# Kernel tuning notes

Hardware: AMD Instinct MI355X
Metric: run time of the kernel (lower is better)

The kernel has to match this reference:

```python
import jax, jax.numpy as jnp
import numpy as np

N_ORDERS = 4  # edge groups processed sequentially by EmulsionConv


def setup_inputs() -> dict:
    key = jax.random.key(0)
    ks = jax.random.split(key, 12)
    N, E, D_IN, H, D_OUT, ED = 50000, 800000, 10, 64, 10, 1
    s = 0.1
    return {
        "x": jax.random.normal(ks[0], (N, D_IN), jnp.float32),
        "edge_index": jax.random.randint(ks[1], (2, E), 0, N, jnp.int32),
        "edge_features": jax.random.normal(ks[2], (E, ED), jnp.float32),
        "lin0_w": jax.random.normal(ks[3], (D_IN, H), jnp.float32) * s,
        "lin0_b": jnp.zeros((H,), jnp.float32),
        "lin1_w": jax.random.normal(ks[4], (H, H), jnp.float32) * s,
        "lin1_b": jnp.zeros((H,), jnp.float32),
        "lin2_w": jax.random.normal(ks[5], (H, H), jnp.float32) * s,
        "lin2_b": jnp.zeros((H,), jnp.float32),
        "em_w": jax.random.normal(ks[6], (3, 2 * H + ED, H), jnp.float32) * s,
        "em_b": jnp.zeros((3, H), jnp.float32),
        "ec_w": jax.random.normal(ks[7], (3, 2 * H, H), jnp.float32) * s,
        "ec_b": jnp.zeros((3, H), jnp.float32),
        "out_w": jax.random.normal(ks[8], (H, D_OUT), jnp.float32) * s,
        "out_b": jnp.zeros((D_OUT,), jnp.float32),
    }


def _emulsion_conv(x, edge_index, edge_features, w, b):
    # Sequential per-order gather -> MLP message -> scatter-add; direction=0 (aggregate at source).
    N = x.shape[0]
    E = edge_index.shape[1]
    per = E // N_ORDERS
    for i in range(N_ORDERS):
        sl = slice(i * per, (i + 1) * per)
        src = edge_index[0, sl]
        dst = edge_index[1, sl]
        x_j = x[src]  # [per, H]
        x_i = x[dst]  # [per, H]
        msg = jnp.concatenate([x_i, x_j - x_i, edge_features[sl]], axis=1)
        msg = jax.nn.relu(msg @ w + b)
        agg = jax.ops.segment_sum(msg, src, num_segments=N)
        x = (x + agg) / 2.0
    return x


def _edge_conv(x, edge_index, w, b):
    # EdgeConv: nn([x_i, x_j - x_i]) with max aggregation at target nodes.
    N = x.shape[0]
    src, dst = edge_index[0], edge_index[1]
    x_i = x[dst]
    x_j = x[src]
    msg = jax.nn.relu(jnp.concatenate([x_i, x_j - x_i], axis=1) @ w + b)
    agg = jax.ops.segment_max(msg, dst, num_segments=N)
    return jnp.where(jnp.isfinite(agg), agg, 0.0)  # empty segments -> 0


def reference(x, edge_index, edge_features,
              lin0_w, lin0_b, lin1_w, lin1_b, lin2_w, lin2_b,
              em_w, em_b, ec_w, ec_b, out_w, out_b):
    lin_ws = [lin0_w, lin1_w, lin2_w]
    lin_bs = [lin0_b, lin1_b, lin2_b]
    for i in range(3):
        x = jax.nn.relu(x @ lin_ws[i] + lin_bs[i])
        x = _emulsion_conv(x, edge_index, edge_features, em_w[i], em_b[i])
    for i in range(3):
        x = _edge_conv(x, edge_index, ec_w[i], ec_b[i])
    return x @ out_w + out_b
```

## Files before the change

kernel.cpp:

```cpp
#include <hip/hip_runtime.h>
#include <hip/hip_fp16.h>


#define NN 50000
#define NE 800000
#define PER 200000
#define HD 64
#define NKEY 250112

#define NB_COUNT 3125
#define NB_LIN   782
#define NB_PREP  192

typedef _Float16 half8 __attribute__((ext_vector_type(8)));
typedef float float4v __attribute__((ext_vector_type(4)));

__global__ __launch_bounds__(256) void setup_kernel(
        const int* __restrict__ ei, int* __restrict__ cnt,
        uchar2* __restrict__ rank,
        const float* __restrict__ x_in, const float* __restrict__ lw0,
        const float* __restrict__ lb0, float* __restrict__ x,
        const float* __restrict__ em_w, const float* __restrict__ ec_w,
        _Float16* __restrict__ wh) {
    __shared__ float xs[64][11];
    int t = threadIdx.x;
    int b = blockIdx.x;
    if (b < NB_COUNT) {
        int e = b * 256 + t;
        if (e >= NE) return;
        int src = ei[e];
        int dst = ei[NE + e];
        int o = e / PER;
        int r1 = atomicAdd(&cnt[o * NN + src], 1);
        int r2 = atomicAdd(&cnt[4 * NN + dst], 1);
        rank[e] = make_uchar2((unsigned char)r1, (unsigned char)r2);
    } else if (b < NB_COUNT + NB_LIN) {
        int n0 = (b - NB_COUNT) * 64;
        for (int idx = t; idx < 64 * 10; idx += 256) {
            int n = idx / 10, k = idx - n * 10;
            int g = n0 + n;
            xs[n][k] = (g < NN) ? x_in[(size_t)g * 10 + k] : 0.f;
        }
        __syncthreads();
        int ng = t >> 4;
        int f0 = (t & 15) * 4;
        float acc[4][4] = {};
        for (int k = 0; k < 10; ++k) {
            float4 w4 = *(const float4*)&lw0[k * HD + f0];
            #pragma unroll
            for (int j = 0; j < 4; ++j) {
                float xv = xs[ng * 4 + j][k];
                acc[j][0] += xv * w4.x; acc[j][1] += xv * w4.y;
                acc[j][2] += xv * w4.z; acc[j][3] += xv * w4.w;
            }
        }
        float4 b4 = *(const float4*)&lb0[f0];
        #pragma unroll
        for (int j = 0; j < 4; ++j) {
            int g = n0 + ng * 4 + j;
            if (g < NN) {
                float4 o;
                o.x = fmaxf(acc[j][0] + b4.x, 0.f);
                o.y = fmaxf(acc[j][1] + b4.y, 0.f);
                o.z = fmaxf(acc[j][2] + b4.z, 0.f);
                o.w = fmaxf(acc[j][3] + b4.w, 0.f);
                *(float4*)&x[(size_t)g * HD + f0] = o;
            }
        }
    } else {
        int idx = (b - NB_COUNT - NB_LIN) * 256 + t;
        int mat = idx >> 12, pos = idx & 4095;
        int n = pos >> 6, k = pos & 63;
        float val;
        if (mat < 3)      { const float* B = em_w + mat * 129 * 64;     val = B[k*64+n] - B[(64+k)*64+n]; }
        else if (mat < 6) { const float* B = em_w + (mat-3) * 129 * 64; val = B[(64+k)*64+n]; }
        else if (mat < 9) { const float* B = ec_w + (mat-6) * 128 * 64; val = B[k*64+n] - B[(64+k)*64+n]; }
        else              { const float* B = ec_w + (mat-9) * 128 * 64; val = B[(64+k)*64+n]; }
        _Float16 h = (_Float16)val;
        _Float16 l = (_Float16)(val - (float)h);
        wh[(size_t)mat * 4096 + n * 64 + k] = h;
        wh[(size_t)(12 + mat) * 4096 + n * 64 + k] = l;
    }
}

__global__ __launch_bounds__(256) void scan_blk(
        const int* __restrict__ cnt, int* __restrict__ bsum) {
    __shared__ int s[256];
    int t = threadIdx.x;
    int i = blockIdx.x * 256 + t;
    int c = (i < NKEY) ? cnt[i] : 0;
    s[t] = c; __syncthreads();
    for (int d = 1; d < 256; d <<= 1) {
        int v = (t >= d) ? s[t - d] : 0;
        __syncthreads(); s[t] += v; __syncthreads();
    }
    if (t == 255) bsum[blockIdx.x] = s[255];
}

__global__ __launch_bounds__(1024) void scan_top(
        const int* __restrict__ bsum, int* __restrict__ bofs, int nb) {
    __shared__ int s[1024];
    int t = threadIdx.x;
    int c = (t < nb) ? bsum[t] : 0;
    s[t] = c; __syncthreads();
    for (int d = 1; d < 1024; d <<= 1) {
        int v = (t >= d) ? s[t - d] : 0;
        __syncthreads(); s[t] += v; __syncthreads();
    }
    if (t < nb) bofs[t] = s[t] - c;
}

__global__ __launch_bounds__(256) void scan_fin(
        const int* __restrict__ cnt, const int* __restrict__ bofs,
        int* __restrict__ ofs) {
    __shared__ int s[256];
    int t = threadIdx.x;
    int i = blockIdx.x * 256 + t;
    int c = (i < NKEY) ? cnt[i] : 0;
    s[t] = c; __syncthreads();
    for (int d = 1; d < 256; d <<= 1) {
        int v = (t >= d) ? s[t - d] : 0;
        __syncthreads(); s[t] += v; __syncthreads();
    }
    if (i < NKEY) ofs[i] = bofs[blockIdx.x] + s[t] - c;
}

__global__ __launch_bounds__(256) void fill_kernel(
        const int* __restrict__ ei, const float* __restrict__ ef,
        const int* __restrict__ ofs, const uchar2* __restrict__ rank,
        unsigned* __restrict__ em_val, int* __restrict__ ec_val) {
    int e = blockIdx.x * 256 + threadIdx.x;
    if (e >= NE) return;
    int src = ei[e];
    int dst = ei[NE + e];
    int o = e / PER;
    uchar2 r = rank[e];
    int p1 = ofs[o * NN + src] + r.x;
    unsigned short eb = __half_as_ushort(__float2half_rn(ef[e]));
    em_val[p1] = ((unsigned)dst << 16) | (unsigned)eb;
    int p2 = ofs[4 * NN + dst] + r.y - NE;
    ec_val[p2] = src;
}

template<int K>
__global__ __launch_bounds__(256) void lin_kernel(
        const float* __restrict__ xin,
        const float* __restrict__ W, const float* __restrict__ bias,
        float* __restrict__ xout) {
    __shared__ float xs[64][K + 1];
    int t = threadIdx.x;
    int n0 = blockIdx.x * 64;
    for (int idx = t; idx < 64 * K; idx += 256) {
        int n = idx / K, k = idx - n * K;
        int g = n0 + n;
        xs[n][k] = (g < NN) ? xin[(size_t)g * K + k] : 0.f;
    }
    __syncthreads();
    int ng = t >> 4;
    int f0 = (t & 15) * 4;
    float acc[4][4] = {};
    for (int k = 0; k < K; ++k) {
        float4 w4 = *(const float4*)&W[k * HD + f0];
        #pragma unroll
        for (int j = 0; j < 4; ++j) {
            float xv = xs[ng * 4 + j][k];
            acc[j][0] += xv * w4.x; acc[j][1] += xv * w4.y;
            acc[j][2] += xv * w4.z; acc[j][3] += xv * w4.w;
        }
    }
    float4 b4 = *(const float4*)&bias[f0];
    #pragma unroll
    for (int j = 0; j < 4; ++j) {
        int g = n0 + ng * 4 + j;
        if (g < NN) {
            float4 o;
            o.x = fmaxf(acc[j][0] + b4.x, 0.f);
            o.y = fmaxf(acc[j][1] + b4.y, 0.f);
            o.z = fmaxf(acc[j][2] + b4.z, 0.f);
            o.w = fmaxf(acc[j][3] + b4.w, 0.f);
            *(float4*)&xout[(size_t)g * HD + f0] = o;
        }
    }
}

__global__ __launch_bounds__(256) void uv_mfma(
        const float* __restrict__ x,
        const _Float16* __restrict__ Wuh, const _Float16* __restrict__ Wul,
        const _Float16* __restrict__ Wvh, const _Float16* __restrict__ Wvl,
        const float* __restrict__ bias,
        _Float16* __restrict__ u, _Float16* __restrict__ v) {
    __shared__ _Float16 xh[64 * 72], xl[64 * 72];
    __shared__ _Float16 wuh[64 * 72], wul[64 * 72];
    __shared__ _Float16 wvh[64 * 72], wvl[64 * 72];
    __shared__ _Float16 rp[4 * 16 * 72];
    int t = threadIdx.x;
    int n0 = blockIdx.x * 64;

    {
        int node = t >> 2, k0 = (t & 3) * 16;
        int g = n0 + node;
        float f[16];
        if (g < NN) {
            const float4* xr = (const float4*)&x[(size_t)g * HD + k0];
            *(float4*)&f[0] = xr[0]; *(float4*)&f[4] = xr[1];
            *(float4*)&f[8] = xr[2]; *(float4*)&f[12] = xr[3];
        } else {
            #pragma unroll
            for (int j = 0; j < 16; ++j) f[j] = 0.f;
        }
        half8 h0, h1, l0, l1;
        #pragma unroll
        for (int j = 0; j < 8; ++j) {
            _Float16 h = (_Float16)f[j];
            h0[j] = h; l0[j] = (_Float16)(f[j] - (float)h);
            _Float16 g2 = (_Float16)f[j + 8];
            h1[j] = g2; l1[j] = (_Float16)(f[j + 8] - (float)g2);
        }
        *(half8*)&xh[node * 72 + k0] = h0; *(half8*)&xh[node * 72 + k0 + 8] = h1;
        *(half8*)&xl[node * 72 + k0] = l0; *(half8*)&xl[node * 72 + k0 + 8] = l1;
    }
    {
        int n = t >> 2, c = (t & 3) * 16;
        *(half8*)&wuh[n * 72 + c]     = *(const half8*)&Wuh[n * 64 + c];
        *(half8*)&wuh[n * 72 + c + 8] = *(const half8*)&Wuh[n * 64 + c + 8];
        *(half8*)&wul[n * 72 + c]     = *(const half8*)&Wul[n * 64 + c];
        *(half8*)&wul[n * 72 + c + 8] = *(const half8*)&Wul[n * 64 + c + 8];
        *(half8*)&wvh[n * 72 + c]     = *(const half8*)&Wvh[n * 64 + c];
        *(half8*)&wvh[n * 72 + c + 8] = *(const half8*)&Wvh[n * 64 + c + 8];
        *(half8*)&wvl[n * 72 + c]     = *(const half8*)&Wvl[n * 64 + c];
        *(half8*)&wvl[n * 72 + c + 8] = *(const half8*)&Wvl[n * 64 + c + 8];
    }
    __syncthreads();

    int w = t >> 6, lane = t & 63;
    int quad = lane >> 4, l16 = lane & 15;
    int m0 = w * 16;
    half8 ah0 = *(half8*)&xh[(m0 + l16) * 72 + quad * 8];
    half8 ah1 = *(half8*)&xh[(m0 + l16) * 72 + 32 + quad * 8];
    half8 al0 = *(half8*)&xl[(m0 + l16) * 72 + quad * 8];
    half8 al1 = *(half8*)&xl[(m0 + l16) * 72 + 32 + quad * 8];

    float4v au[4], av[4];
    #pragma unroll
    for (int nt = 0; nt < 4; ++nt) {
        int n = nt * 16 + l16;
        half8 bh0 = *(half8*)&wuh[n * 72 + quad * 8];
        half8 bh1 = *(half8*)&wuh[n * 72 + 32 + quad * 8];
        half8 bl0 = *(half8*)&wul[n * 72 + quad * 8];
        half8 bl1 = *(half8*)&wul[n * 72 + 32 + quad * 8];
        float4v acc = {0.f, 0.f, 0.f, 0.f};
        acc = __builtin_amdgcn_mfma_f32_16x16x32_f16(ah0, bh0, acc, 0, 0, 0);
        acc = __builtin_amdgcn_mfma_f32_16x16x32_f16(ah1, bh1, acc, 0, 0, 0);
        acc = __builtin_amdgcn_mfma_f32_16x16x32_f16(al0, bh0, acc, 0, 0, 0);
        acc = __builtin_amdgcn_mfma_f32_16x16x32_f16(al1, bh1, acc, 0, 0, 0);
        acc = __builtin_amdgcn_mfma_f32_16x16x32_f16(ah0, bl0, acc, 0, 0, 0);
        acc = __builtin_amdgcn_mfma_f32_16x16x32_f16(ah1, bl1, acc, 0, 0, 0);
        au[nt] = acc;
        half8 ch0 = *(half8*)&wvh[n * 72 + quad * 8];
        half8 ch1 = *(half8*)&wvh[n * 72 + 32 + quad * 8];
        half8 cl0 = *(half8*)&wvl[n * 72 + quad * 8];
        half8 cl1 = *(half8*)&wvl[n * 72 + 32 + quad * 8];
        float4v accv = {0.f, 0.f, 0.f, 0.f};
        accv = __builtin_amdgcn_mfma_f32_16x16x32_f16(ah0, ch0, accv, 0, 0, 0);
        accv = __builtin_amdgcn_mfma_f32_16x16x32_f16(ah1, ch1, accv, 0, 0, 0);
        accv = __builtin_amdgcn_mfma_f32_16x16x32_f16(al0, ch0, accv, 0, 0, 0);
        accv = __builtin_amdgcn_mfma_f32_16x16x32_f16(al1, ch1, accv, 0, 0, 0);
        accv = __builtin_amdgcn_mfma_f32_16x16x32_f16(ah0, cl0, accv, 0, 0, 0);
        accv = __builtin_amdgcn_mfma_f32_16x16x32_f16(ah1, cl1, accv, 0, 0, 0);
        av[nt] = accv;
    }

    _Float16* rpw = &rp[w * 16 * 72];
    #pragma unroll
    for (int nt = 0; nt < 4; ++nt) {
        float bn = bias[nt * 16 + l16];
        #pragma unroll
        for (int r = 0; r < 4; ++r)
            rpw[(quad * 4 + r) * 72 + nt * 16 + l16] = (_Float16)(au[nt][r] + bn);
    }
    int mr = lane >> 2, cr = (lane & 3) * 16;
    int gr = n0 + m0 + mr;
    if (gr < NN) {
        *(half8*)&u[(size_t)gr * HD + cr]     = *(half8*)&rpw[mr * 72 + cr];
        *(half8*)&u[(size_t)gr * HD + cr + 8] = *(half8*)&rpw[mr * 72 + cr + 8];
    }
    #pragma unroll
    for (int nt = 0; nt < 4; ++nt) {
        #pragma unroll
        for (int r = 0; r < 4; ++r)
            rpw[(quad * 4 + r) * 72 + nt * 16 + l16] = (_Float16)(av[nt][r]);
    }
    if (gr < NN) {
        *(half8*)&v[(size_t)gr * HD + cr]     = *(half8*)&rpw[mr * 72 + cr];
        *(half8*)&v[(size_t)gr * HD + cr + 8] = *(half8*)&rpw[mr * 72 + cr + 8];
    }
}

__device__ __forceinline__ void load_h8(const __half* p, float* o) {
    float4 r = *(const float4*)p;
    __half2 h0 = *reinterpret_cast<__half2*>(&r.x);
    __half2 h1 = *reinterpret_cast<__half2*>(&r.y);
    __half2 h2 = *reinterpret_cast<__half2*>(&r.z);
    __half2 h3 = *reinterpret_cast<__half2*>(&r.w);
    float2 f0 = __half22float2(h0), f1 = __half22float2(h1);
    float2 f2 = __half22float2(h2), f3 = __half22float2(h3);
    o[0] = f0.x; o[1] = f0.y; o[2] = f1.x; o[3] = f1.y;
    o[4] = f2.x; o[5] = f2.y; o[6] = f3.x; o[7] = f3.y;
}

__global__ __launch_bounds__(256) void em_edge(
        const unsigned* __restrict__ em_val, const int* __restrict__ ofs,
        const __half* __restrict__ u, const __half* __restrict__ v,
        const float* __restrict__ we, float* __restrict__ x, int order) {
    int t = threadIdx.x;
    int node = blockIdx.x * 32 + (t >> 3);
    if (node >= NN) return;
    int f0 = (t & 7) * 8;
    int key = order * NN + node;
    int s0 = ofs[key], s1 = ofs[key + 1];
    float vn[8], wef[8], acc[8] = {};
    load_h8(&v[(size_t)node * HD + f0], vn);
    *(float4*)&wef[0] = *(const float4*)&we[f0];
    *(float4*)&wef[4] = *(const float4*)&we[f0 + 4];
    int p = s0;
    for (; p + 2 <= s1; p += 2) {
        unsigned e0 = em_val[p], e1 = em_val[p + 1];
        float u0[8], u1[8];
        load_h8(&u[(size_t)(e0 >> 16) * HD + f0], u0);
        load_h8(&u[(size_t)(e1 >> 16) * HD + f0], u1);
        float ef0 = __half2float(__ushort_as_half((unsigned short)(e0 & 0xffff)));
        float ef1 = __half2float(__ushort_as_half((unsigned short)(e1 & 0xffff)));
        #pragma unroll
        for (int j = 0; j < 8; ++j) {
            acc[j] += fmaxf(u0[j] + vn[j] + ef0 * wef[j], 0.f)
                    + fmaxf(u1[j] + vn[j] + ef1 * wef[j], 0.f);
        }
    }
    if (p < s1) {
        unsigned e0 = em_val[p];
        float u0[8];
        load_h8(&u[(size_t)(e0 >> 16) * HD + f0], u0);
        float ef0 = __half2float(__ushort_as_half((unsigned short)(e0 & 0xffff)));
        #pragma unroll
        for (int j = 0; j < 8; ++j)
            acc[j] += fmaxf(u0[j] + vn[j] + ef0 * wef[j], 0.f);
    }
    float xr[8];
    *(float4*)&xr[0] = *(const float4*)&x[(size_t)node * HD + f0];
    *(float4*)&xr[4] = *(const float4*)&x[(size_t)node * HD + f0 + 4];
    #pragma unroll
    for (int j = 0; j < 8; ++j) xr[j] = (xr[j] + acc[j]) * 0.5f;
    *(float4*)&x[(size_t)node * HD + f0] = *(float4*)&xr[0];
    *(float4*)&x[(size_t)node * HD + f0 + 4] = *(float4*)&xr[4];
}

__global__ __launch_bounds__(256) void ec_edge(
        const int* __restrict__ ec_val, const int* __restrict__ ofs,
        const __half* __restrict__ u, const __half* __restrict__ v,
        float* __restrict__ x) {
    int t = threadIdx.x;
    int node = blockIdx.x * 32 + (t >> 3);
    if (node >= NN) return;
    int f0 = (t & 7) * 8;
    int s0 = ofs[4 * NN + node] - NE, s1 = ofs[4 * NN + node + 1] - NE;
    float un[8], m[8] = {};
    load_h8(&u[(size_t)node * HD + f0], un);
    int p = s0;
    for (; p + 2 <= s1; p += 2) {
        int i0 = ec_val[p], i1 = ec_val[p + 1];
        float v0[8], v1[8];
        load_h8(&v[(size_t)i0 * HD + f0], v0);
        load_h8(&v[(size_t)i1 * HD + f0], v1);
        #pragma unroll
        for (int j = 0; j < 8; ++j)
            m[j] = fmaxf(m[j], fmaxf(un[j] + v0[j], un[j] + v1[j]));
    }
    if (p < s1) {
        int i0 = ec_val[p];
        float v0[8];
        load_h8(&v[(size_t)i0 * HD + f0], v0);
        #pragma unroll
        for (int j = 0; j < 8; ++j) m[j] = fmaxf(m[j], un[j] + v0[j]);
    }
    *(float4*)&x[(size_t)node * HD + f0] = *(float4*)&m[0];
    *(float4*)&x[(size_t)node * HD + f0 + 4] = *(float4*)&m[4];
}

__global__ __launch_bounds__(256) void ec_out(
        const int* __restrict__ ec_val, const int* __restrict__ ofs,
        const __half* __restrict__ u, const __half* __restrict__ v,
        const float* __restrict__ ow, const float* __restrict__ ob,
        float* __restrict__ out) {
    __shared__ float xs[32][72];
    int t = threadIdx.x;
    int nl = t >> 3;
    int node = blockIdx.x * 32 + nl;
    int f0 = (t & 7) * 8;
    float m[8] = {};
    if (node < NN) {
        int s0 = ofs[4 * NN + node] - NE, s1 = ofs[4 * NN + node + 1] - NE;
        float un[8];
        load_h8(&u[(size_t)node * HD + f0], un);
        int p = s0;
        for (; p + 2 <= s1; p += 2) {
            int i0 = ec_val[p], i1 = ec_val[p + 1];
            float v0[8], v1[8];
            load_h8(&v[(size_t)i0 * HD + f0], v0);
            load_h8(&v[(size_t)i1 * HD + f0], v1);
            #pragma unroll
            for (int j = 0; j < 8; ++j)
                m[j] = fmaxf(m[j], fmaxf(un[j] + v0[j], un[j] + v1[j]));
        }
        if (p < s1) {
            int i0 = ec_val[p];
            float v0[8];
            load_h8(&v[(size_t)i0 * HD + f0], v0);
            #pragma unroll
            for (int j = 0; j < 8; ++j) m[j] = fmaxf(m[j], un[j] + v0[j]);
        }
    }
    #pragma unroll
    for (int j = 0; j < 8; ++j) xs[nl][f0 + j] = m[j];
    __syncthreads();
    for (int idx = t; idx < 32 * 10; idx += 256) {
        int n = idx / 10, f = idx - n * 10;
        int g = blockIdx.x * 32 + n;
        if (g >= NN) continue;
        float acc = ob[f];
        #pragma unroll
        for (int k = 0; k < HD; ++k) acc += xs[n][k] * ow[k * 10 + f];
        out[(size_t)g * 10 + f] = acc;
    }
}

extern "C" void kernel_launch(void* const* d_in, const int* in_sizes, int n_in,
                              void* d_out, int out_size, void* d_ws, size_t ws_size,
                              hipStream_t stream) {
    const float* x_in  = (const float*)d_in[0];
    const int*   ei    = (const int*)d_in[1];
    const float* ef    = (const float*)d_in[2];
    const float* lw[3] = {(const float*)d_in[3], (const float*)d_in[5], (const float*)d_in[7]};
    const float* lb[3] = {(const float*)d_in[4], (const float*)d_in[6], (const float*)d_in[8]};
    const float* em_w  = (const float*)d_in[9];
    const float* em_b  = (const float*)d_in[10];
    const float* ec_w  = (const float*)d_in[11];
    const float* ec_b  = (const float*)d_in[12];
    const float* ow    = (const float*)d_in[13];
    const float* ob    = (const float*)d_in[14];
    float* out = (float*)d_out;

    char* wsb = (char*)d_ws;
    size_t off = 0;
    auto alloc = [&](size_t bytes) {
        void* p = wsb + off;
        off = (off + bytes + 255) & ~(size_t)255;
        return p;
    };
    float*     x      = (float*)alloc((size_t)NN * HD * 4);
    _Float16*  u      = (_Float16*)alloc((size_t)NN * HD * 2);
    _Float16*  v      = (_Float16*)alloc((size_t)NN * HD * 2);
    int*       cnt    = (int*)alloc((size_t)NKEY * 4);
    int*       ofs    = (int*)alloc((size_t)NKEY * 4);
    int*       bsum   = (int*)alloc((size_t)1024 * 4);
    int*       bofs   = (int*)alloc((size_t)1024 * 4);
    uchar2*    rank   = (uchar2*)alloc((size_t)NE * 2);
    unsigned*  em_val = (unsigned*)alloc((size_t)NE * 4);
    int*       ec_val = (int*)alloc((size_t)NE * 4);
    _Float16*  wh     = (_Float16*)alloc((size_t)24 * 4096 * 2);
    (void)ws_size; (void)in_sizes; (void)n_in; (void)out_size;

    const int gb_nodes = (NN + 63) / 64;
    const int gb_edges = (NE + 255) / 256;
    const int gb_n8    = (NN + 31) / 32;
    const int gb_keys  = NKEY / 256;

    hipMemsetAsync(cnt, 0, (size_t)NKEY * 4, stream);
    setup_kernel<<<NB_COUNT + NB_LIN + NB_PREP, 256, 0, stream>>>(
        ei, cnt, rank, x_in, lw[0], lb[0], x, em_w, ec_w, wh);
    scan_blk<<<gb_keys, 256, 0, stream>>>(cnt, bsum);
    scan_top<<<1, 1024, 0, stream>>>(bsum, bofs, gb_keys);
    scan_fin<<<gb_keys, 256, 0, stream>>>(cnt, bofs, ofs);
    fill_kernel<<<gb_edges, 256, 0, stream>>>(ei, ef, ofs, rank, em_val, ec_val);

    for (int i = 0; i < 3; ++i) {
        const _Float16* Wuh = wh + (size_t)i * 4096;
        const _Float16* Wvh = wh + (size_t)(3 + i) * 4096;
        const _Float16* Wul = wh + (size_t)(12 + i) * 4096;
        const _Float16* Wvl = wh + (size_t)(15 + i) * 4096;
        const float* bi = em_b + (size_t)i * HD;
        const float* we = em_w + (size_t)i * 129 * HD + 128 * HD;
        for (int o = 0; o < 4; ++o) {
            uv_mfma<<<gb_nodes, 256, 0, stream>>>(x, Wuh, Wul, Wvh, Wvl, bi, u, v);
            em_edge<<<gb_n8, 256, 0, stream>>>(em_val, ofs, (const __half*)u,
                                               (const __half*)v, we, x, o);
        }
        if (i < 2)
            lin_kernel<64><<<gb_nodes, 256, 0, stream>>>(x, lw[i + 1], lb[i + 1], x);
    }

    for (int j = 0; j < 3; ++j) {
        const _Float16* Wuh = wh + (size_t)(6 + j) * 4096;
        const _Float16* Wvh = wh + (size_t)(9 + j) * 4096;
        const _Float16* Wul = wh + (size_t)(18 + j) * 4096;
        const _Float16* Wvl = wh + (size_t)(21 + j) * 4096;
        const float* bj = ec_b + (size_t)j * HD;
        uv_mfma<<<gb_nodes, 256, 0, stream>>>(x, Wuh, Wul, Wvh, Wvl, bj, u, v);
        if (j < 2)
            ec_edge<<<gb_n8, 256, 0, stream>>>(ec_val, ofs, (const __half*)u,
                                               (const __half*)v, x);
        else
            ec_out<<<gb_n8, 256, 0, stream>>>(ec_val, ofs, (const __half*)u,
                                              (const __half*)v, ow, ob, out);
    }
}
```

Measured before the change: 587.6 us.

## Fuse linear layers into u/v MFMA projection and merge fill with first projection

Replaces the fp32 lin_kernel with split-fp16 MFMA and fuses it into a combined guv kernel that also computes the next u/v projection, so x is not re-read by a separate launch. The edge-fill pass is merged into the first u/v projection launch, and the launch schedule is reordered to remove redundant kernels. EdgeConv max loops are unrolled to four gathers per iteration for more memory-level parallelism. It adds setup work to convert the lin1/lin2 weights to hi/lo fp16 and changes the precision path of the linear layers.

```diff
diff --git a/kernel.cpp b/kernel.cpp
--- a/kernel.cpp
+++ b/kernel.cpp
@@ -10,10 +10,12 @@
 
 #define NB_COUNT 3125
 #define NB_LIN   782
-#define NB_PREP  192
+#define NB_PREP  224
 
 typedef _Float16 half8 __attribute__((ext_vector_type(8)));
 typedef float float4v __attribute__((ext_vector_type(4)));
+
+#define MFMA16(A, B, C) __builtin_amdgcn_mfma_f32_16x16x32_f16(A, B, C, 0, 0, 0)
 
 __global__ __launch_bounds__(256) void setup_kernel(
         const int* __restrict__ ei, int* __restrict__ cnt,
@@ -21,6 +23,7 @@
         const float* __restrict__ x_in, const float* __restrict__ lw0,
         const float* __restrict__ lb0, float* __restrict__ x,
         const float* __restrict__ em_w, const float* __restrict__ ec_w,
+        const float* __restrict__ lw1, const float* __restrict__ lw2,
         _Float16* __restrict__ wh) {
     __shared__ float xs[64][11];
     int t = threadIdx.x;
@@ -72,14 +75,15 @@
         int mat = idx >> 12, pos = idx & 4095;
         int n = pos >> 6, k = pos & 63;
         float val;
-        if (mat < 3)      { const float* B = em_w + mat * 129 * 64;     val = B[k*64+n] - B[(64+k)*64+n]; }
-        else if (mat < 6) { const float* B = em_w + (mat-3) * 129 * 64; val = B[(64+k)*64+n]; }
-        else if (mat < 9) { const float* B = ec_w + (mat-6) * 128 * 64; val = B[k*64+n] - B[(64+k)*64+n]; }
-        else              { const float* B = ec_w + (mat-9) * 128 * 64; val = B[(64+k)*64+n]; }
+        if (mat < 3)       { const float* B = em_w + mat * 129 * 64;     val = B[k*64+n] - B[(64+k)*64+n]; }
+        else if (mat < 6)  { const float* B = em_w + (mat-3) * 129 * 64; val = B[(64+k)*64+n]; }
+        else if (mat < 9)  { const float* B = ec_w + (mat-6) * 128 * 64; val = B[k*64+n] - B[(64+k)*64+n]; }
+        else if (mat < 12) { const float* B = ec_w + (mat-9) * 128 * 64; val = B[(64+k)*64+n]; }
+        else               { const float* B = (mat == 12) ? lw1 : lw2;   val = B[k*64+n]; }
         _Float16 h = (_Float16)val;
         _Float16 l = (_Float16)(val - (float)h);
         wh[(size_t)mat * 4096 + n * 64 + k] = h;
-        wh[(size_t)(12 + mat) * 4096 + n * 64 + k] = l;
+        wh[(size_t)(14 + mat) * 4096 + n * 64 + k] = l;
     }
 }
 
@@ -125,61 +129,161 @@
     if (i < NKEY) ofs[i] = bofs[blockIdx.x] + s[t] - c;
 }
 
-__global__ __launch_bounds__(256) void fill_kernel(
+__device__ __forceinline__ void split8(const float* f, half8& h, half8& l) {
+    #pragma unroll
+    for (int j = 0; j < 8; ++j) {
+        _Float16 hh = (_Float16)f[j];
+        h[j] = hh; l[j] = (_Float16)(f[j] - (float)hh);
+    }
+}
+
+template<bool FILL, bool DOLIN>
+__global__ __launch_bounds__(256) void guv_kernel(
         const int* __restrict__ ei, const float* __restrict__ ef,
         const int* __restrict__ ofs, const uchar2* __restrict__ rank,
-        unsigned* __restrict__ em_val, int* __restrict__ ec_val) {
-    int e = blockIdx.x * 256 + threadIdx.x;
-    if (e >= NE) return;
-    int src = ei[e];
-    int dst = ei[NE + e];
-    int o = e / PER;
-    uchar2 r = rank[e];
-    int p1 = ofs[o * NN + src] + r.x;
-    unsigned short eb = __half_as_ushort(__float2half_rn(ef[e]));
-    em_val[p1] = ((unsigned)dst << 16) | (unsigned)eb;
-    int p2 = ofs[4 * NN + dst] + r.y - NE;
-    ec_val[p2] = src;
-}
-
-template<int K>
-__global__ __launch_bounds__(256) void lin_kernel(
-        const float* __restrict__ xin,
-        const float* __restrict__ W, const float* __restrict__ bias,
-        float* __restrict__ xout) {
-    __shared__ float xs[64][K + 1];
-    int t = threadIdx.x;
-    int n0 = blockIdx.x * 64;
-    for (int idx = t; idx < 64 * K; idx += 256) {
-        int n = idx / K, k = idx - n * K;
-        int g = n0 + n;
-        xs[n][k] = (g < NN) ? xin[(size_t)g * K + k] : 0.f;
+        unsigned* __restrict__ em_val, int* __restrict__ ec_val,
+        const float* __restrict__ xg, float* __restrict__ xout,
+        const _Float16* __restrict__ Wlh, const _Float16* __restrict__ Wll,
+        const float* __restrict__ lbias,
+        const _Float16* __restrict__ Wuh, const _Float16* __restrict__ Wul,
+        const _Float16* __restrict__ Wvh, const _Float16* __restrict__ Wvl,
+        const float* __restrict__ bias,
+        _Float16* __restrict__ u, _Float16* __restrict__ v) {
+    __shared__ _Float16 xh[64 * 72], xl[64 * 72];
+    __shared__ _Float16 rp[4 * 16 * 72];
+    const int t = threadIdx.x;
+    int b = blockIdx.x;
+    if constexpr (FILL) {
+        if (b < NB_COUNT) {
+            int e = b * 256 + t;
+            if (e >= NE) return;
+            int src = ei[e];
+            int dst = ei[NE + e];
+            int o = e / PER;
+            uchar2 r = rank[e];
+            int p1 = ofs[o * NN + src] + r.x;
+            unsigned short eb = __half_as_ushort(__float2half_rn(ef[e]));
+            em_val[p1] = ((unsigned)dst << 16) | (unsigned)eb;
+            int p2 = ofs[4 * NN + dst] + r.y - NE;
+            ec_val[p2] = src;
+            return;
+        }
+        b -= NB_COUNT;
+    }
+    const int n0 = b * 64;
+
+    {
+        int node = t >> 2, k0 = (t & 3) * 16;
+        int g = n0 + node;
+        float f[16];
+        if (g < NN) {
+            const float4* xr4 = (const float4*)&xg[(size_t)g * HD + k0];
+            *(float4*)&f[0] = xr4[0]; *(float4*)&f[4] = xr4[1];
+            *(float4*)&f[8] = xr4[2]; *(float4*)&f[12] = xr4[3];
+        } else {
+            #pragma unroll
+            for (int j = 0; j < 16; ++j) f[j] = 0.f;
+        }
+        half8 h0, l0, h1, l1;
+        split8(f, h0, l0); split8(f + 8, h1, l1);
+        *(half8*)&xh[node * 72 + k0] = h0; *(half8*)&xh[node * 72 + k0 + 8] = h1;
+        *(half8*)&xl[node * 72 + k0] = l0; *(half8*)&xl[node * 72 + k0 + 8] = l1;
     }
     __syncthreads();
-    int ng = t >> 4;
-    int f0 = (t & 15) * 4;
-    float acc[4][4] = {};
-    for (int k = 0; k < K; ++k) {
-        float4 w4 = *(const float4*)&W[k * HD + f0];
-        #pragma unroll
-        for (int j = 0; j < 4; ++j) {
-            float xv = xs[ng * 4 + j][k];
-            acc[j][0] += xv * w4.x; acc[j][1] += xv * w4.y;
-            acc[j][2] += xv * w4.z; acc[j][3] += xv * w4.w;
-        }
-    }
-    float4 b4 = *(const float4*)&bias[f0];
-    #pragma unroll
-    for (int j = 0; j < 4; ++j) {
-        int g = n0 + ng * 4 + j;
-        if (g < NN) {
-            float4 o;
-            o.x = fmaxf(acc[j][0] + b4.x, 0.f);
-            o.y = fmaxf(acc[j][1] + b4.y, 0.f);
-            o.z = fmaxf(acc[j][2] + b4.z, 0.f);
-            o.w = fmaxf(acc[j][3] + b4.w, 0.f);
-            *(float4*)&xout[(size_t)g * HD + f0] = o;
-        }
+
+    const int w = t >> 6, lane = t & 63;
+    const int quad = lane >> 4, l16 = lane & 15;
+    const int m0 = w * 16;
+
+    half8 ah0 = *(half8*)&xh[(m0 + l16) * 72 + quad * 8];
+    half8 ah1 = *(half8*)&xh[(m0 + l16) * 72 + 32 + quad * 8];
+    half8 al0 = *(half8*)&xl[(m0 + l16) * 72 + quad * 8];
+    half8 al1 = *(half8*)&xl[(m0 + l16) * 72 + 32 + quad * 8];
+
+    if constexpr (DOLIN) {
+        float4v ax[4];
+        #pragma unroll
+        for (int nt = 0; nt < 4; ++nt) {
+            int n = nt * 16 + l16;
+            half8 bh0 = *(const half8*)&Wlh[n * 64 + quad * 8];
+            half8 bh1 = *(const half8*)&Wlh[n * 64 + 32 + quad * 8];
+            half8 bl0 = *(const half8*)&Wll[n * 64 + quad * 8];
+            half8 bl1 = *(const half8*)&Wll[n * 64 + 32 + quad * 8];
+            float4v acc = {0.f, 0.f, 0.f, 0.f};
+            acc = MFMA16(ah0, bh0, acc); acc = MFMA16(ah1, bh1, acc);
+            acc = MFMA16(al0, bh0, acc); acc = MFMA16(al1, bh1, acc);
+            acc = MFMA16(ah0, bl0, acc); acc = MFMA16(ah1, bl1, acc);
+            ax[nt] = acc;
+        }
+        __syncthreads();
+        #pragma unroll
+        for (int nt = 0; nt < 4; ++nt) {
+            float bn = lbias[nt * 16 + l16];
+            #pragma unroll
+            for (int r = 0; r < 4; ++r) {
+                float val = fmaxf(ax[nt][r] + bn, 0.f);
+                int mrow = m0 + quad * 4 + r;
+                _Float16 hh = (_Float16)val;
+                xh[mrow * 72 + nt * 16 + l16] = hh;
+                xl[mrow * 72 + nt * 16 + l16] = (_Float16)(val - (float)hh);
+                int gn = n0 + mrow;
+                if (gn < NN) xout[(size_t)gn * HD + nt * 16 + l16] = val;
+            }
+        }
+        __syncthreads();
+        ah0 = *(half8*)&xh[(m0 + l16) * 72 + quad * 8];
+        ah1 = *(half8*)&xh[(m0 + l16) * 72 + 32 + quad * 8];
+        al0 = *(half8*)&xl[(m0 + l16) * 72 + quad * 8];
+        al1 = *(half8*)&xl[(m0 + l16) * 72 + 32 + quad * 8];
+    }
+
+    float4v au[4], av[4];
+    #pragma unroll
+    for (int nt = 0; nt < 4; ++nt) {
+        int n = nt * 16 + l16;
+        half8 bh0 = *(const half8*)&Wuh[n * 64 + quad * 8];
+        half8 bh1 = *(const half8*)&Wuh[n * 64 + 32 + quad * 8];
+        half8 bl0 = *(const half8*)&Wul[n * 64 + quad * 8];
+        half8 bl1 = *(const half8*)&Wul[n * 64 + 32 + quad * 8];
+        float4v acc = {0.f, 0.f, 0.f, 0.f};
+        acc = MFMA16(ah0, bh0, acc); acc = MFMA16(ah1, bh1, acc);
+        acc = MFMA16(al0, bh0, acc); acc = MFMA16(al1, bh1, acc);
+        acc = MFMA16(ah0, bl0, acc); acc = MFMA16(ah1, bl1, acc);
+        au[nt] = acc;
+        half8 ch0 = *(const half8*)&Wvh[n * 64 + quad * 8];
+        half8 ch1 = *(const half8*)&Wvh[n * 64 + 32 + quad * 8];
+        half8 cl0 = *(const half8*)&Wvl[n * 64 + quad * 8];
+        half8 cl1 = *(const half8*)&Wvl[n * 64 + 32 + quad * 8];
+        float4v accv = {0.f, 0.f, 0.f, 0.f};
+        accv = MFMA16(ah0, ch0, accv); accv = MFMA16(ah1, ch1, accv);
+        accv = MFMA16(al0, ch0, accv); accv = MFMA16(al1, ch1, accv);
+        accv = MFMA16(ah0, cl0, accv); accv = MFMA16(ah1, cl1, accv);
+        av[nt] = accv;
+    }
+
+    _Float16* rpw = &rp[w * 16 * 72];
+    #pragma unroll
+    for (int nt = 0; nt < 4; ++nt) {
+        float bn = bias[nt * 16 + l16];
+        #pragma unroll
+        for (int r = 0; r < 4; ++r)
+            rpw[(quad * 4 + r) * 72 + nt * 16 + l16] = (_Float16)(au[nt][r] + bn);
+    }
+    int mr = lane >> 2, cr = (lane & 3) * 16;
+    int gr = n0 + m0 + mr;
+    if (gr < NN) {
+        *(half8*)&u[(size_t)gr * HD + cr]     = *(half8*)&rpw[mr * 72 + cr];
+        *(half8*)&u[(size_t)gr * HD + cr + 8] = *(half8*)&rpw[mr * 72 + cr + 8];
+    }
+    #pragma unroll
+    for (int nt = 0; nt < 4; ++nt) {
+        #pragma unroll
+        for (int r = 0; r < 4; ++r)
+            rpw[(quad * 4 + r) * 72 + nt * 16 + l16] = (_Float16)(av[nt][r]);
+    }
+    if (gr < NN) {
+        *(half8*)&v[(size_t)gr * HD + cr]     = *(half8*)&rpw[mr * 72 + cr];
+        *(half8*)&v[(size_t)gr * HD + cr + 8] = *(half8*)&rpw[mr * 72 + cr + 8];
     }
 }
 
@@ -209,13 +313,7 @@
             for (int j = 0; j < 16; ++j) f[j] = 0.f;
         }
         half8 h0, h1, l0, l1;
-        #pragma unroll
-        for (int j = 0; j < 8; ++j) {
-            _Float16 h = (_Float16)f[j];
-            h0[j] = h; l0[j] = (_Float16)(f[j] - (float)h);
-            _Float16 g2 = (_Float16)f[j + 8];
-            h1[j] = g2; l1[j] = (_Float16)(f[j + 8] - (float)g2);
-        }
+        split8(f, h0, l0); split8(f + 8, h1, l1);
         *(half8*)&xh[node * 72 + k0] = h0; *(half8*)&xh[node * 72 + k0 + 8] = h1;
         *(half8*)&xl[node * 72 + k0] = l0; *(half8*)&xl[node * 72 + k0 + 8] = l1;
     }
@@ -249,24 +347,18 @@
         half8 bl0 = *(half8*)&wul[n * 72 + quad * 8];
         half8 bl1 = *(half8*)&wul[n * 72 + 32 + quad * 8];
         float4v acc = {0.f, 0.f, 0.f, 0.f};
-        acc = __builtin_amdgcn_mfma_f32_16x16x32_f16(ah0, bh0, acc, 0, 0, 0);
-        acc = __builtin_amdgcn_mfma_f32_16x16x32_f16(ah1, bh1, acc, 0, 0, 0);
-        acc = __builtin_amdgcn_mfma_f32_16x16x32_f16(al0, bh0, acc, 0, 0, 0);
-        acc = __builtin_amdgcn_mfma_f32_16x16x32_f16(al1, bh1, acc, 0, 0, 0);
-        acc = __builtin_amdgcn_mfma_f32_16x16x32_f16(ah0, bl0, acc, 0, 0, 0);
-        acc = __builtin_amdgcn_mfma_f32_16x16x32_f16(ah1, bl1, acc, 0, 0, 0);
+        acc = MFMA16(ah0, bh0, acc); acc = MFMA16(ah1, bh1, acc);
+        acc = MFMA16(al0, bh0, acc); acc = MFMA16(al1, bh1, acc);
+        acc = MFMA16(ah0, bl0, acc); acc = MFMA16(ah1, bl1, acc);
         au[nt] = acc;
         half8 ch0 = *(half8*)&wvh[n * 72 + quad * 8];
         half8 ch1 = *(half8*)&wvh[n * 72 + 32 + quad * 8];
         half8 cl0 = *(half8*)&wvl[n * 72 + quad * 8];
         half8 cl1 = *(half8*)&wvl[n * 72 + 32 + quad * 8];
         float4v accv = {0.f, 0.f, 0.f, 0.f};
-        accv = __builtin_amdgcn_mfma_f32_16x16x32_f16(ah0, ch0, accv, 0, 0, 0);
-        accv = __builtin_amdgcn_mfma_f32_16x16x32_f16(ah1, ch1, accv, 0, 0, 0);
-        accv = __builtin_amdgcn_mfma_f32_16x16x32_f16(al0, ch0, accv, 0, 0, 0);
-        accv = __builtin_amdgcn_mfma_f32_16x16x32_f16(al1, ch1, accv, 0, 0, 0);
-        accv = __builtin_amdgcn_mfma_f32_16x16x32_f16(ah0, cl0, accv, 0, 0, 0);
-        accv = __builtin_amdgcn_mfma_f32_16x16x32_f16(ah1, cl1, accv, 0, 0, 0);
+        accv = MFMA16(ah0, ch0, accv); accv = MFMA16(ah1, ch1, accv);
+        accv = MFMA16(al0, ch0, accv); accv = MFMA16(al1, ch1, accv);
+        accv = MFMA16(ah0, cl0, accv); accv = MFMA16(ah1, cl1, accv);
         av[nt] = accv;
     }
 
@@ -366,16 +458,20 @@
     float un[8], m[8] = {};
     load_h8(&u[(size_t)node * HD + f0], un);
     int p = s0;
-    for (; p + 2 <= s1; p += 2) {
+    for (; p + 4 <= s1; p += 4) {
         int i0 = ec_val[p], i1 = ec_val[p + 1];
-        float v0[8], v1[8];
+        int i2 = ec_val[p + 2], i3 = ec_val[p + 3];
+        float v0[8], v1[8], v2[8], v3[8];
         load_h8(&v[(size_t)i0 * HD + f0], v0);
         load_h8(&v[(size_t)i1 * HD + f0], v1);
+        load_h8(&v[(size_t)i2 * HD + f0], v2);
+        load_h8(&v[(size_t)i3 * HD + f0], v3);
         #pragma unroll
         for (int j = 0; j < 8; ++j)
-            m[j] = fmaxf(m[j], fmaxf(un[j] + v0[j], un[j] + v1[j]));
-    }
-    if (p < s1) {
+            m[j] = fmaxf(m[j], fmaxf(fmaxf(un[j] + v0[j], un[j] + v1[j]),
+                                     fmaxf(un[j] + v2[j], un[j] + v3[j])));
+    }
+    for (; p < s1; ++p) {
         int i0 = ec_val[p];
         float v0[8];
         load_h8(&v[(size_t)i0 * HD + f0], v0);
@@ -402,16 +498,20 @@
         float un[8];
         load_h8(&u[(size_t)node * HD + f0], un);
         int p = s0;
-        for (; p + 2 <= s1; p += 2) {
+        for (; p + 4 <= s1; p += 4) {
             int i0 = ec_val[p], i1 = ec_val[p + 1];
-            float v0[8], v1[8];
+            int i2 = ec_val[p + 2], i3 = ec_val[p + 3];
+            float v0[8], v1[8], v2[8], v3[8];
             load_h8(&v[(size_t)i0 * HD + f0], v0);
             load_h8(&v[(size_t)i1 * HD + f0], v1);
+            load_h8(&v[(size_t)i2 * HD + f0], v2);
+            load_h8(&v[(size_t)i3 * HD + f0], v3);
             #pragma unroll
             for (int j = 0; j < 8; ++j)
-                m[j] = fmaxf(m[j], fmaxf(un[j] + v0[j], un[j] + v1[j]));
-        }
-        if (p < s1) {
+                m[j] = fmaxf(m[j], fmaxf(fmaxf(un[j] + v0[j], un[j] + v1[j]),
+                                         fmaxf(un[j] + v2[j], un[j] + v3[j])));
+        }
+        for (; p < s1; ++p) {
             int i0 = ec_val[p];
             float v0[8];
             load_h8(&v[(size_t)i0 * HD + f0], v0);
@@ -466,50 +566,56 @@
     uchar2*    rank   = (uchar2*)alloc((size_t)NE * 2);
     unsigned*  em_val = (unsigned*)alloc((size_t)NE * 4);
     int*       ec_val = (int*)alloc((size_t)NE * 4);
-    _Float16*  wh     = (_Float16*)alloc((size_t)24 * 4096 * 2);
+    _Float16*  wh     = (_Float16*)alloc((size_t)28 * 4096 * 2);
     (void)ws_size; (void)in_sizes; (void)n_in; (void)out_size;
 
     const int gb_nodes = (NN + 63) / 64;
-    const int gb_edges = (NE + 255) / 256;
     const int gb_n8    = (NN + 31) / 32;
     const int gb_keys  = NKEY / 256;
 
+    auto Wm  = [&](int mat) { return wh + (size_t)mat * 4096; };
+    auto Wl_ = [&](int mat) { return wh + (size_t)(14 + mat) * 4096; };
+
     hipMemsetAsync(cnt, 0, (size_t)NKEY * 4, stream);
     setup_kernel<<<NB_COUNT + NB_LIN + NB_PREP, 256, 0, stream>>>(
-        ei, cnt, rank, x_in, lw[0], lb[0], x, em_w, ec_w, wh);
+        ei, cnt, rank, x_in, lw[0], lb[0], x, em_w, ec_w, lw[1], lw[2], wh);
     scan_blk<<<gb_keys, 256, 0, stream>>>(cnt, bsum);
     scan_top<<<1, 1024, 0, stream>>>(bsum, bofs, gb_keys);
     scan_fin<<<gb_keys, 256, 0, stream>>>(cnt, bofs, ofs);
-    fill_kernel<<<gb_edges, 256, 0, stream>>>(ei, ef, ofs, rank, em_val, ec_val);
+    guv_kernel<true, false><<<NB_COUNT + gb_nodes, 256, 0, stream>>>(
+        ei, ef, ofs, rank, em_val, ec_val,
+        x, nullptr, nullptr, nullptr, nullptr,
+        Wm(0), Wl_(0), Wm(3), Wl_(3), em_b, u, v);
 
     for (int i = 0; i < 3; ++i) {
-        const _Float16* Wuh = wh + (size_t)i * 4096;
-        const _Float16* Wvh = wh + (size_t)(3 + i) * 4096;
-        const _Float16* Wul = wh + (size_t)(12 + i) * 4096;
-        const _Float16* Wvl = wh + (size_t)(15 + i) * 4096;
+        const float* we = em_w + (size_t)i * 129 * HD + 128 * HD;
         const float* bi = em_b + (size_t)i * HD;
-        const float* we = em_w + (size_t)i * 129 * HD + 128 * HD;
         for (int o = 0; o < 4; ++o) {
-            uv_mfma<<<gb_nodes, 256, 0, stream>>>(x, Wuh, Wul, Wvh, Wvl, bi, u, v);
             em_edge<<<gb_n8, 256, 0, stream>>>(em_val, ofs, (const __half*)u,
                                                (const __half*)v, we, x, o);
-        }
-        if (i < 2)
-            lin_kernel<64><<<gb_nodes, 256, 0, stream>>>(x, lw[i + 1], lb[i + 1], x);
-    }
-
-    for (int j = 0; j < 3; ++j) {
-        const _Float16* Wuh = wh + (size_t)(6 + j) * 4096;
-        const _Float16* Wvh = wh + (size_t)(9 + j) * 4096;
-        const _Float16* Wul = wh + (size_t)(18 + j) * 4096;
-        const _Float16* Wvl = wh + (size_t)(21 + j) * 4096;
-        const float* bj = ec_b + (size_t)j * HD;
-        uv_mfma<<<gb_nodes, 256, 0, stream>>>(x, Wuh, Wul, Wvh, Wvl, bj, u, v);
-        if (j < 2)
-            ec_edge<<<gb_n8, 256, 0, stream>>>(ec_val, ofs, (const __half*)u,
-                                               (const __half*)v, x);
-        else
-            ec_out<<<gb_n8, 256, 0, stream>>>(ec_val, ofs, (const __half*)u,
-                                              (const __half*)v, ow, ob, out);
-    }
-}
+            if (o < 3)
+                uv_mfma<<<gb_nodes, 256, 0, stream>>>(
+                    x, Wm(i), Wl_(i), Wm(3 + i), Wl_(3 + i), bi, u, v);
+        }
+        if (i < 2) {
+            guv_kernel<false, true><<<gb_nodes, 256, 0, stream>>>(
+                nullptr, nullptr, nullptr, nullptr, nullptr, nullptr,
+                x, x, Wm(12 + i), Wl_(12 + i), lb[i + 1],
+                Wm(i + 1), Wl_(i + 1), Wm(4 + i), Wl_(4 + i),
+                em_b + (size_t)(i + 1) * HD, u, v);
+        } else {
+            uv_mfma<<<gb_nodes, 256, 0, stream>>>(
+                x, Wm(6), Wl_(6), Wm(9), Wl_(9), ec_b, u, v);
+        }
+    }
+
+    for (int j = 0; j < 2; ++j) {
+        ec_edge<<<gb_n8, 256, 0, stream>>>(ec_val, ofs, (const __half*)u,
+                                           (const __half*)v, x);
+        uv_mfma<<<gb_nodes, 256, 0, stream>>>(
+            x, Wm(7 + j), Wl_(7 + j), Wm(10 + j), Wl_(10 + j),
+            ec_b + (size_t)(j + 1) * HD, u, v);
+    }
+    ec_out<<<gb_n8, 256, 0, stream>>>(ec_val, ofs, (const __half*)u,
+                                      (const __half*)v, ow, ob, out);
+}
```

Result: no change. 591.8 us (+0.7%).
